# Kernel optimization log

Hardware: AMD Instinct MI355X
Metric: run time of the kernel (lower is better)

Reference implementation:

```python
import jax, jax.numpy as jnp
import numpy as np

HIDDEN = 256

def setup_inputs() -> dict:
    key = jax.random.key(0)
    k1, k2, k3, k4, k5 = jax.random.split(key, 5)
    hidden = jax.random.normal(k1, (1, 32, HIDDEN), dtype=jnp.float32)
    encoder_outputs = jax.random.normal(k2, (32, 8192, HIDDEN), dtype=jnp.float32)
    # nn.Linear(hidden*2, hidden): weight (H, 2H), bias (H,)
    W = jax.random.normal(k3, (HIDDEN, 2 * HIDDEN), dtype=jnp.float32) / np.sqrt(2 * HIDDEN)
    b = jax.random.normal(k4, (HIDDEN,), dtype=jnp.float32) * 0.01
    v = jax.random.uniform(k5, (HIDDEN,), dtype=jnp.float32)
    return {"hidden": hidden, "encoder_outputs": encoder_outputs, "W": W, "b": b, "v": v}

def reference(hidden, encoder_outputs, W, b, v):
    # hidden: (1, B, H) -> (B, 1, H); avoid materializing the concat by
    # splitting Linear(2H->H) into two matmuls (same math as cat + Linear).
    Wh, We = W[:, :HIDDEN], W[:, HIDDEN:]          # each (H, 2H/2)
    h = jnp.transpose(hidden, (1, 0, 2))           # (B, 1, H)
    # (B,1,H)@(H,H)^T broadcasts over seq; (B,S,H)@(H,H)^T
    pre = jnp.einsum('boh,kh->bok', h, Wh) + jnp.einsum('bsh,kh->bsk', encoder_outputs, We) + b
    scores = jnp.tanh(pre)                          # (B, S, H)
    logits = jnp.einsum('bsh,h->bs', scores, v)     # (B, S)
    attn_weights = jax.nn.softmax(logits, axis=1)   # (B, S)
    context = jnp.einsum('bs,bsh->bh', attn_weights, encoder_outputs)  # (B, H)
    return (context, attn_weights)
```

## Files before the change

### kernel.cpp

```cpp
#include <hip/hip_runtime.h>


typedef _Float16 f16x8 __attribute__((ext_vector_type(8)));
typedef float    f32x4 __attribute__((ext_vector_type(4)));

__device__ __forceinline__ float fast_tanh(float x){
  x = fminf(15.f, fmaxf(-15.f, x));
  float e = __expf(2.f * x);
  return (e - 1.f) * __builtin_amdgcn_rcpf(e + 1.f);
}

__global__ void prep_kernel(const float* __restrict__ hidden, const float* __restrict__ W,
                            const float* __restrict__ bias, _Float16* __restrict__ Bfrag,
                            float* __restrict__ qb)
{
  int blk = blockIdx.x;
  if (blk < 256){
    int tid  = blk * 256 + threadIdx.x;
    int j    = tid & 7;
    int lane = (tid >> 3) & 63;
    int kc   = (tid >> 9) & 7;
    int nt   = tid >> 12;
    int lc   = lane & 15, q = lane >> 4;
    int row  = nt * 16 + lc;
    int col  = 256 + kc * 32 + q * 8 + j;
    Bfrag[tid] = (_Float16)W[row * 512 + col];
  } else {
    int b = blk - 256;
    int k = threadIdx.x;
    const float4* hp = (const float4*)(hidden + b * 256);
    const float4* wp = (const float4*)(W + k * 512);
    float s = 0.f;
    for (int i = 0; i < 64; i++){
      float4 h4 = hp[i], w4 = wp[i];
      s += h4.x * w4.x + h4.y * w4.y + h4.z * w4.z + h4.w * w4.w;
    }
    qb[b * 256 + k] = s + bias[k];
  }
}

__global__ __launch_bounds__(256) void attn_main(
    const float* __restrict__ enc, const _Float16* __restrict__ Bfrag,
    const float* __restrict__ qb, const float* __restrict__ v,
    float* __restrict__ logits, float* __restrict__ P,
    float* __restrict__ mw, float* __restrict__ lw)
{
  __shared__ _Float16 Bs[8192];
  __shared__ float sl[64];
  __shared__ float Pl[256];

  const int b = blockIdx.x >> 7, chunk = blockIdx.x & 127;
  const int tid = threadIdx.x, wv = tid >> 6, lane = tid & 63;
  const int q = lane >> 4, lc = lane & 15;
  const int rowBase = b * 8192 + chunk * 64;
  const int waveRow = wv * 16;

  Pl[tid] = 0.f;

  f16x8 A[8];
  {
    const float* rp = enc + (size_t)(rowBase + waveRow + lc) * 256 + q * 8;
    #pragma unroll
    for (int kc = 0; kc < 8; kc++){
      const float4* p = (const float4*)(rp + kc * 32);
      float4 x0 = p[0], x1 = p[1];
      f16x8 af;
      af[0] = (_Float16)x0.x; af[1] = (_Float16)x0.y; af[2] = (_Float16)x0.z; af[3] = (_Float16)x0.w;
      af[4] = (_Float16)x1.x; af[5] = (_Float16)x1.y; af[6] = (_Float16)x1.z; af[7] = (_Float16)x1.w;
      A[kc] = af;
    }
  }

  float plog[4] = {0, 0, 0, 0};
  const float* qbB = qb + b * 256;

  for (int h = 0; h < 8; h++){
    __syncthreads();
    {
      const f16x8* src = (const f16x8*)(Bfrag + h * 8192);
      f16x8* dst = (f16x8*)Bs;
      #pragma unroll
      for (int i = 0; i < 4; i++) dst[tid + i * 256] = src[tid + i * 256];
    }
    __syncthreads();
    #pragma unroll
    for (int ntl = 0; ntl < 2; ntl++){
      const int nt = h * 2 + ntl;
      f32x4 acc = {0, 0, 0, 0};
      const f16x8* bp = ((const f16x8*)Bs) + ntl * 512 + lane;
      #pragma unroll
      for (int kc = 0; kc < 8; kc++){
        f16x8 bf = bp[kc * 64];
        acc = __builtin_amdgcn_mfma_f32_16x16x32_f16(A[kc], bf, acc, 0, 0, 0);
      }
      const int col = nt * 16 + lc;
      const float qv = qbB[col], vv = v[col];
      #pragma unroll
      for (int r = 0; r < 4; r++)
        plog[r] += fast_tanh(acc[r] + qv) * vv;
    }
  }

  #pragma unroll
  for (int r = 0; r < 4; r++){
    float s = plog[r];
    s += __shfl_xor(s, 1); s += __shfl_xor(s, 2);
    s += __shfl_xor(s, 4); s += __shfl_xor(s, 8);
    plog[r] = s;
  }
  if (lc == 0){
    #pragma unroll
    for (int r = 0; r < 4; r++){
      int rl = waveRow + q * 4 + r;
      sl[rl] = plog[r];
      logits[rowBase + rl] = plog[r];
    }
  }
  __syncthreads();

  if (tid < 64){
    float x = sl[tid];
    float m = x;
    for (int o = 1; o < 64; o <<= 1) m = fmaxf(m, __shfl_xor(m, o));
    float e = __expf(x - m);
    sl[tid] = e;
    float s2 = e;
    for (int o = 1; o < 64; o <<= 1) s2 += __shfl_xor(s2, o);
    if (tid == 0){ mw[blockIdx.x] = m; lw[blockIdx.x] = s2; }
  }
  __syncthreads();

  const float w0 = sl[waveRow + lc];
  #pragma unroll
  for (int kc = 0; kc < 8; kc++){
    float c8[8];
    #pragma unroll
    for (int j = 0; j < 8; j++)
      c8[j] = w0 * (float)A[kc][j];
    #pragma unroll
    for (int j = 0; j < 8; j++){
      float s = c8[j];
      s += __shfl_xor(s, 1); s += __shfl_xor(s, 2);
      s += __shfl_xor(s, 4); s += __shfl_xor(s, 8);
      c8[j] = s;
    }
    if (lc == 0){
      #pragma unroll
      for (int j = 0; j < 8; j++) atomicAdd(&Pl[kc * 32 + q * 8 + j], c8[j]);
    }
  }
  __syncthreads();
  P[(size_t)blockIdx.x * 256 + tid] = Pl[tid];
}

__global__ void attn_finish(const float* __restrict__ logits, const float* __restrict__ P,
                            const float* __restrict__ mw, const float* __restrict__ lw,
                            float* __restrict__ out)
{
  const int b = blockIdx.x, t = threadIdx.x;
  __shared__ float sm[128], sw[128], se[128], sM[1], sL[1];
  if (t < 128){ sm[t] = mw[b * 128 + t]; sw[t] = lw[b * 128 + t]; }
  __syncthreads();
  if (t == 0){
    float M = -1e30f;
    for (int i = 0; i < 128; i++) M = fmaxf(M, sm[i]);
    sM[0] = M;
  }
  __syncthreads();
  const float M = sM[0];
  if (t < 128) se[t] = __expf(sm[t] - M);
  __syncthreads();
  if (t == 0){
    float L = 0.f;
    for (int i = 0; i < 128; i++) L += sw[i] * se[i];
    sL[0] = L;
  }
  __syncthreads();
  const float inv = 1.f / sL[0];
  float c = 0.f;
  for (int ch = 0; ch < 128; ch++) c += se[ch] * P[(size_t)(b * 128 + ch) * 256 + t];
  out[b * 256 + t] = c * inv;
  const float* lg = logits + (size_t)b * 8192;
  float* ao = out + 8192 + (size_t)b * 8192;
  for (int s = t; s < 8192; s += 256) ao[s] = __expf(lg[s] - M) * inv;
}

extern "C" void kernel_launch(void* const* d_in, const int* in_sizes, int n_in,
                              void* d_out, int out_size, void* d_ws, size_t ws_size,
                              hipStream_t stream)
{
  const float* hidden = (const float*)d_in[0];
  const float* enc    = (const float*)d_in[1];
  const float* W      = (const float*)d_in[2];
  const float* bias   = (const float*)d_in[3];
  const float* v      = (const float*)d_in[4];
  float* out = (float*)d_out;

  char* ws = (char*)d_ws;
  _Float16* Bfrag = (_Float16*)ws;
  float* qb     = (float*)(ws + (128 << 10));
  float* logits = (float*)(ws + (160 << 10));
  float* P      = (float*)(ws + (160 << 10) + (1 << 20));
  float* mw     = (float*)(ws + (160 << 10) + (5 << 20));
  float* lw     = (float*)(ws + (160 << 10) + (5 << 20) + (16 << 10));

  prep_kernel<<<288, 256, 0, stream>>>(hidden, W, bias, Bfrag, qb);
  attn_main<<<4096, 256, 0, stream>>>(enc, Bfrag, qb, v, logits, P, mw, lw);
  attn_finish<<<32, 256, 0, stream>>>(logits, P, mw, lw, out);
}
```

Measured before the change: 459.6 us.

## Keep W fragments in registers, stage encoder tile in LDS, re-read for context

Restructures attn_main to 512 threads, where each wave holds two column tiles of the W fragments in registers, and the 64-row encoder tile is converted to fp16 and staged in shared memory. Partial logits are reduced across the eight waves through LDS. The context partial sum is now computed by re-reading the fp32 encoder rows from global memory (expected to hit cache) instead of using shuffle and atomic reductions. This removes the per-iteration B reload and barriers, and the fp16 rounding of the context. The cost is 32KB of LDS per block and a second pass over the encoder tile.

```diff
diff --git a/kernel.cpp b/kernel.cpp
--- a/kernel.cpp
+++ b/kernel.cpp
@@ -2,6 +2,7 @@
 
 
 typedef _Float16 f16x8 __attribute__((ext_vector_type(8)));
+typedef _Float16 f16x4 __attribute__((ext_vector_type(4)));
 typedef float    f32x4 __attribute__((ext_vector_type(4)));
 
 __device__ __forceinline__ float fast_tanh(float x){
@@ -39,118 +40,109 @@
   }
 }
 
-__global__ __launch_bounds__(256) void attn_main(
+__global__ __launch_bounds__(512) void attn_main(
     const float* __restrict__ enc, const _Float16* __restrict__ Bfrag,
     const float* __restrict__ qb, const float* __restrict__ v,
     float* __restrict__ logits, float* __restrict__ P,
     float* __restrict__ mw, float* __restrict__ lw)
 {
-  __shared__ _Float16 Bs[8192];
-  __shared__ float sl[64];
-  __shared__ float Pl[256];
+  __shared__ _Float16 Af[16384];
+  __shared__ float plg[8][64];
+  __shared__ float sw[64];
+  __shared__ float Pl2[2][256];
 
   const int b = blockIdx.x >> 7, chunk = blockIdx.x & 127;
   const int tid = threadIdx.x, wv = tid >> 6, lane = tid & 63;
   const int q = lane >> 4, lc = lane & 15;
   const int rowBase = b * 8192 + chunk * 64;
-  const int waveRow = wv * 16;
-
-  Pl[tid] = 0.f;
-
-  f16x8 A[8];
-  {
-    const float* rp = enc + (size_t)(rowBase + waveRow + lc) * 256 + q * 8;
-    #pragma unroll
-    for (int kc = 0; kc < 8; kc++){
-      const float4* p = (const float4*)(rp + kc * 32);
-      float4 x0 = p[0], x1 = p[1];
-      f16x8 af;
-      af[0] = (_Float16)x0.x; af[1] = (_Float16)x0.y; af[2] = (_Float16)x0.z; af[3] = (_Float16)x0.w;
-      af[4] = (_Float16)x1.x; af[5] = (_Float16)x1.y; af[6] = (_Float16)x1.z; af[7] = (_Float16)x1.w;
-      A[kc] = af;
-    }
-  }
-
-  float plog[4] = {0, 0, 0, 0};
-  const float* qbB = qb + b * 256;
-
-  for (int h = 0; h < 8; h++){
-    __syncthreads();
-    {
-      const f16x8* src = (const f16x8*)(Bfrag + h * 8192);
-      f16x8* dst = (f16x8*)Bs;
+
+  const int nt0 = wv * 2;
+  f16x8 Breg[2][8];
+  {
+    const f16x8* Bsrc = (const f16x8*)Bfrag;
+    #pragma unroll
+    for (int ntl = 0; ntl < 2; ntl++)
       #pragma unroll
-      for (int i = 0; i < 4; i++) dst[tid + i * 256] = src[tid + i * 256];
-    }
-    __syncthreads();
-    #pragma unroll
-    for (int ntl = 0; ntl < 2; ntl++){
-      const int nt = h * 2 + ntl;
-      f32x4 acc = {0, 0, 0, 0};
-      const f16x8* bp = ((const f16x8*)Bs) + ntl * 512 + lane;
+      for (int kc = 0; kc < 8; kc++)
+        Breg[ntl][kc] = Bsrc[((nt0 + ntl) * 8 + kc) * 64 + lane];
+  }
+  float qv[2], vv[2];
+  #pragma unroll
+  for (int ntl = 0; ntl < 2; ntl++){
+    int col = (nt0 + ntl) * 16 + lc;
+    qv[ntl] = qb[b * 256 + col];
+    vv[ntl] = v[col];
+  }
+
+  {
+    const int r = tid >> 3, kc = tid & 7;
+    const float4* src = (const float4*)(enc + (size_t)(rowBase + r) * 256 + kc * 32);
+    const int mt = r >> 4, lcr = r & 15;
+    #pragma unroll
+    for (int i = 0; i < 8; i++){
+      float4 x = src[i];
+      f16x4 h4;
+      h4[0] = (_Float16)x.x; h4[1] = (_Float16)x.y;
+      h4[2] = (_Float16)x.z; h4[3] = (_Float16)x.w;
+      int idx = (((mt * 8 + kc) * 64 + (i >> 1) * 16 + lcr) * 8 + (i & 1) * 4);
+      *(f16x4*)(&Af[idx]) = h4;
+    }
+  }
+  __syncthreads();
+
+  {
+    const f16x8* Afp = (const f16x8*)Af;
+    #pragma unroll
+    for (int mt = 0; mt < 4; mt++){
+      f32x4 acc0 = {0, 0, 0, 0}, acc1 = {0, 0, 0, 0};
       #pragma unroll
       for (int kc = 0; kc < 8; kc++){
-        f16x8 bf = bp[kc * 64];
-        acc = __builtin_amdgcn_mfma_f32_16x16x32_f16(A[kc], bf, acc, 0, 0, 0);
+        f16x8 af = Afp[(mt * 8 + kc) * 64 + lane];
+        acc0 = __builtin_amdgcn_mfma_f32_16x16x32_f16(af, Breg[0][kc], acc0, 0, 0, 0);
+        acc1 = __builtin_amdgcn_mfma_f32_16x16x32_f16(af, Breg[1][kc], acc1, 0, 0, 0);
       }
-      const int col = nt * 16 + lc;
-      const float qv = qbB[col], vv = v[col];
       #pragma unroll
-      for (int r = 0; r < 4; r++)
-        plog[r] += fast_tanh(acc[r] + qv) * vv;
-    }
-  }
-
-  #pragma unroll
-  for (int r = 0; r < 4; r++){
-    float s = plog[r];
-    s += __shfl_xor(s, 1); s += __shfl_xor(s, 2);
-    s += __shfl_xor(s, 4); s += __shfl_xor(s, 8);
-    plog[r] = s;
-  }
-  if (lc == 0){
-    #pragma unroll
-    for (int r = 0; r < 4; r++){
-      int rl = waveRow + q * 4 + r;
-      sl[rl] = plog[r];
-      logits[rowBase + rl] = plog[r];
+      for (int r = 0; r < 4; r++){
+        float s = fast_tanh(acc0[r] + qv[0]) * vv[0] + fast_tanh(acc1[r] + qv[1]) * vv[1];
+        s += __shfl_xor(s, 1); s += __shfl_xor(s, 2);
+        s += __shfl_xor(s, 4); s += __shfl_xor(s, 8);
+        if (lc == 0) plg[wv][mt * 16 + q * 4 + r] = s;
+      }
     }
   }
   __syncthreads();
 
   if (tid < 64){
-    float x = sl[tid];
+    float x = 0.f;
+    #pragma unroll
+    for (int w = 0; w < 8; w++) x += plg[w][tid];
+    logits[rowBase + tid] = x;
     float m = x;
     for (int o = 1; o < 64; o <<= 1) m = fmaxf(m, __shfl_xor(m, o));
     float e = __expf(x - m);
-    sl[tid] = e;
+    sw[tid] = e;
     float s2 = e;
     for (int o = 1; o < 64; o <<= 1) s2 += __shfl_xor(s2, o);
     if (tid == 0){ mw[blockIdx.x] = m; lw[blockIdx.x] = s2; }
   }
   __syncthreads();
 
-  const float w0 = sl[waveRow + lc];
-  #pragma unroll
-  for (int kc = 0; kc < 8; kc++){
-    float c8[8];
-    #pragma unroll
-    for (int j = 0; j < 8; j++)
-      c8[j] = w0 * (float)A[kc][j];
-    #pragma unroll
-    for (int j = 0; j < 8; j++){
-      float s = c8[j];
-      s += __shfl_xor(s, 1); s += __shfl_xor(s, 2);
-      s += __shfl_xor(s, 4); s += __shfl_xor(s, 8);
-      c8[j] = s;
-    }
-    if (lc == 0){
-      #pragma unroll
-      for (int j = 0; j < 8; j++) atomicAdd(&Pl[kc * 32 + q * 8 + j], c8[j]);
-    }
-  }
-  __syncthreads();
-  P[(size_t)blockIdx.x * 256 + tid] = Pl[tid];
+  {
+    const int k = tid & 255, h = tid >> 8;
+    const float* ep = enc + (size_t)(rowBase + h * 32) * 256 + k;
+    const float* swh = sw + h * 32;
+    float s0 = 0.f, s1 = 0.f, s2 = 0.f, s3 = 0.f;
+    #pragma unroll
+    for (int r4 = 0; r4 < 8; r4++){
+      s0 += swh[r4 * 4 + 0] * ep[(size_t)(r4 * 4 + 0) * 256];
+      s1 += swh[r4 * 4 + 1] * ep[(size_t)(r4 * 4 + 1) * 256];
+      s2 += swh[r4 * 4 + 2] * ep[(size_t)(r4 * 4 + 2) * 256];
+      s3 += swh[r4 * 4 + 3] * ep[(size_t)(r4 * 4 + 3) * 256];
+    }
+    Pl2[h][k] = (s0 + s1) + (s2 + s3);
+  }
+  __syncthreads();
+  if (tid < 256) P[(size_t)blockIdx.x * 256 + tid] = Pl2[0][tid] + Pl2[1][tid];
 }
 
 __global__ void attn_finish(const float* __restrict__ logits, const float* __restrict__ P,
@@ -205,6 +197,6 @@
   float* lw     = (float*)(ws + (160 << 10) + (5 << 20) + (16 << 10));
 
   prep_kernel<<<288, 256, 0, stream>>>(hidden, W, bias, Bfrag, qb);
-  attn_main<<<4096, 256, 0, stream>>>(enc, Bfrag, qb, v, logits, P, mw, lw);
+  attn_main<<<4096, 512, 0, stream>>>(enc, Bfrag, qb, v, logits, P, mw, lw);
   attn_finish<<<32, 256, 0, stream>>>(logits, P, mw, lw, out);
 }
```

Result: faster. 414.4 us (-9.8%).
